# Performance work log

Measured on AMD Instinct MI355X. Metric: run time of the kernel, lower is better.

The kernel has to match this reference:

```python
import jax, jax.numpy as jnp
import numpy as np

EPSILON = 0.1       # temperature
ITERATIONS = 10     # Sinkhorn iterations


def setup_inputs() -> dict:
    key = jax.random.key(0)
    z = jax.random.normal(key, (8192, 128), dtype=jnp.float32)  # [2N, D]
    return {"z": z}


def reference(z):
    # L2-normalize rows; cosine similarity of normalized rows is a plain matmul
    z = z / jnp.linalg.norm(z, axis=1, keepdims=True)
    cos_sim = z @ z.T                      # [S, S]
    Cost = 1.0 - cos_sim
    S = Cost.shape[0]
    C = Cost.max()
    eye = jnp.eye(S, dtype=Cost.dtype)
    Cost = C * eye + (1.0 - eye) * Cost    # put max cost on the diagonal
    Probs = jnp.exp(-Cost / EPSILON)
    for _ in range(ITERATIONS):
        Probs = Probs / Probs.sum(axis=1, keepdims=True)   # row normalize
        Probs = (Probs / Probs.sum(axis=0, keepdims=True)).T  # col normalize + transpose (as in source)
    N = S // 2
    Probi = jnp.diagonal(Probs, offset=N)   # positives view1->view2
    Probj = jnp.diagonal(Probs, offset=-N)  # positives view2->view1
    L = -(jnp.log(Probi).sum() + jnp.log(Probj).sum()) / (2 * N)
    return L
```

## Files before the change

kernel.cpp:

```cpp
#include <hip/hip_runtime.h>

#define S_DIM 8192
#define NTRI 2080
#define NWORK 544

typedef __attribute__((ext_vector_type(8))) short short8v;
typedef __attribute__((ext_vector_type(16))) float f32x16;
typedef __attribute__((ext_vector_type(2))) float f32x2;

__device__ inline unsigned short f32_to_bf16(float f) {
    unsigned int b = __builtin_bit_cast(unsigned int, f);
    unsigned int lsb = (b >> 16) & 1u;
    b += 0x7fffu + lsb;
    return (unsigned short)(b >> 16);
}
__device__ inline unsigned int fkey(float f) {
    unsigned int b = __builtin_bit_cast(unsigned int, f);
    return (b & 0x80000000u) ? ~b : (b | 0x80000000u);
}
__device__ inline float fkey_inv(unsigned int k) {
    unsigned int b = (k & 0x80000000u) ? (k & 0x7FFFFFFFu) : ~k;
    return __builtin_bit_cast(float, b);
}

__device__ inline unsigned int f32_to_fp8_scalar(float f) {
#if __has_builtin(__builtin_amdgcn_cvt_pk_fp8_f32)
    return (unsigned int)__builtin_amdgcn_cvt_pk_fp8_f32(f, f, 0, false) & 0xFFu;
#else
    if (f < 0.015625f) return (unsigned int)__float2int_rn(f * 512.0f);
    unsigned int b = __builtin_bit_cast(unsigned int, f);
    unsigned int r = b + 0x7FFFFu + ((b >> 20) & 1u);
    return (r >> 20) - 960u;
#endif
}
__device__ inline unsigned int pack_fp8x4(float a, float b, float c, float d) {
#if __has_builtin(__builtin_amdgcn_cvt_pk_fp8_f32)
    int w = __builtin_amdgcn_cvt_pk_fp8_f32(a, b, 0, false);
    w = __builtin_amdgcn_cvt_pk_fp8_f32(c, d, w, true);
    return (unsigned int)w;
#else
    return f32_to_fp8_scalar(a) | (f32_to_fp8_scalar(b) << 8) |
           (f32_to_fp8_scalar(c) << 16) | (f32_to_fp8_scalar(d) << 24);
#endif
}
#if !__has_builtin(__builtin_amdgcn_cvt_pk_f32_fp8)
__device__ inline float fp8_byte_to_f32(unsigned int u) {
    unsigned int e = (u >> 3) & 15u, m = u & 7u;
    if (e == 0) return (float)m * 0x1p-9f;
    return __builtin_bit_cast(float, ((e + 120u) << 23) | (m << 20));
}
#endif
__device__ inline void fp8x4_to_f32(unsigned int d, float* o) {
#if __has_builtin(__builtin_amdgcn_cvt_pk_f32_fp8)
    f32x2 lo = __builtin_amdgcn_cvt_pk_f32_fp8((int)d, false);
    f32x2 hi = __builtin_amdgcn_cvt_pk_f32_fp8((int)d, true);
    o[0] = lo[0]; o[1] = lo[1]; o[2] = hi[0]; o[3] = hi[1];
#else
    o[0] = fp8_byte_to_f32(d & 0xFFu);
    o[1] = fp8_byte_to_f32((d >> 8) & 0xFFu);
    o[2] = fp8_byte_to_f32((d >> 16) & 0xFFu);
    o[3] = fp8_byte_to_f32((d >> 24) & 0xFFu);
#endif
}

__device__ inline void tri_map(int id, int& bi, int& bj) {
    int j = (int)((sqrtf(8.0f * (float)id + 1.0f) - 1.0f) * 0.5f);
    while ((j + 1) * (j + 2) / 2 <= id) ++j;
    while (j * (j + 1) / 2 > id) --j;
    bj = j;
    bi = id - j * (j + 1) / 2;
}
__device__ inline void work_map(int id, int& R, int& s) {
    int g = (int)((sqrtf(1.0f + 2.0f * (float)id) - 1.0f) * 0.5f);
    while (2 * (g + 1) * (g + 2) <= id) ++g;
    while (2 * g * (g + 1) > id) --g;
    int rem = id - 2 * g * (g + 1);
    int r = rem / (g + 1);
    s = rem - r * (g + 1);
    R = 4 * g + r;
}

__global__ __launch_bounds__(64) void normalize_kernel(const float* __restrict__ z,
                                                       unsigned int* __restrict__ znb,
                                                       float* __restrict__ y0,
                                                       float* __restrict__ y1,
                                                       unsigned int* __restrict__ minslot,
                                                       float* __restrict__ lossacc,
                                                       unsigned int* __restrict__ cnt) {
    int row = blockIdx.x;
    int t = threadIdx.x;
    float2 val = ((const float2*)(z + (size_t)row * 128))[t];
    float ss = val.x * val.x + val.y * val.y;
    #pragma unroll
    for (int off = 32; off; off >>= 1) ss += __shfl_xor(ss, off);
    float inv = 1.0f / sqrtf(ss);
    float2 o; o.x = val.x * inv; o.y = val.y * inv;
    unsigned int pk = (unsigned int)f32_to_bf16(o.x) | ((unsigned int)f32_to_bf16(o.y) << 16);
    znb[((row >> 5) * 512 + (t >> 2) * 32 + (row & 31)) * 4 + (t & 3)] = pk;
    if (t == 0) {
        y0[row] = 1.0f;
        y1[row] = 0.0f;
        if (row == 0) { *minslot = 0xFFFFFFFFu; *lossacc = 0.0f; *cnt = 0u; }
    }
}

__global__ __launch_bounds__(512, 4) void gemm_exp_mfma(const short* __restrict__ znb,
                                                        unsigned char* __restrict__ K8,
                                                        unsigned int* __restrict__ minslot,
                                                        float* __restrict__ lossacc) {
    __shared__ unsigned int Tl[128 * 32];
    __shared__ float wmins[8];
    int bi, bj;
    tri_map(blockIdx.x, bi, bj);
    const bool pairblk = (bj - bi == 32);
    const bool diagblk = (bi == bj);
    const int t = threadIdx.x;
    const int lane = t & 63, w = t >> 6;
    const int tr = w >> 1, tc = w & 1;
    const int cl = lane & 31, hi = lane >> 5;
    const int rowA = bi * 128 + tr * 32;
    const short8v* Z = (const short8v*)znb;

    f32x16 acc[2];
    #pragma unroll
    for (int tj = 0; tj < 2; ++tj)
        #pragma unroll
        for (int e = 0; e < 16; ++e) acc[tj][e] = 0.0f;

    #pragma unroll
    for (int step = 0; step < 8; ++step) {
        const int chunk = step * 2 + hi;
        short8v af = Z[(rowA >> 5) * 512 + chunk * 32 + cl];
        short8v bf[2];
        #pragma unroll
        for (int tj = 0; tj < 2; ++tj) {
            int rB = bj * 128 + tc * 64 + tj * 32;
            bf[tj] = Z[(rB >> 5) * 512 + chunk * 32 + cl];
        }
        #pragma unroll
        for (int tj = 0; tj < 2; ++tj)
            acc[tj] = __builtin_amdgcn_mfma_f32_32x32x16_bf16(af, bf[tj], acc[tj], 0, 0, 0);
    }

    float mn = 3.0e38f;
    float pl = 0.0f;
    #pragma unroll
    for (int tj = 0; tj < 2; ++tj) {
        int colL = tc * 64 + tj * 32 + cl;
        int colG = bj * 128 + colL;
        int gswz = ((colL & 15) << 1) | ((colL >> 3) & 1);
        #pragma unroll
        for (int g = 0; g < 4; ++g) {
            int rowG = rowA + 8 * g + 4 * hi;
            float ev[4];
            #pragma unroll
            for (int kk = 0; kk < 4; ++kk) {
                float c = acc[tj][g * 4 + kk];
                mn = fminf(mn, c);
                if (pairblk && (colG - rowG - kk) == 4096) pl += 20.0f * (c - 1.0f);
                ev[kk] = __expf(10.0f * fminf(c, 0.6f));
            }
            if (diagblk) {
                #pragma unroll
                for (int kk = 0; kk < 4; ++kk)
                    if (rowG + kk == colG) ev[kk] = 0.0f;
            }
            unsigned int wv = pack_fp8x4(ev[0], ev[1], ev[2], ev[3]);
            int r4b = tr * 8 + 2 * g + hi;
            Tl[colL * 32 + (r4b ^ gswz)] = wv;
        }
    }
    #pragma unroll
    for (int off = 32; off; off >>= 1) mn = fminf(mn, __shfl_xor(mn, off));
    if (lane == 0) wmins[w] = mn;
    if (pairblk) {
        #pragma unroll
        for (int off = 32; off; off >>= 1) pl += __shfl_xor(pl, off);
        if (lane == 0) atomicAdd(lossacc, pl);
    }
    __syncthreads();
    if (t == 0) {
        float bmin = wmins[0];
        #pragma unroll
        for (int k = 1; k < 8; ++k) bmin = fminf(bmin, wmins[k]);
        atomicMin(minslot, fkey(bmin));
    }

    const size_t gbase = (size_t)(bj * 128) * S_DIM + (size_t)bi * 128;
    #pragma unroll
    for (int it = 0; it < 2; ++it) {
        int c = it * 64 + (t >> 3);
        int dq = (t & 7) * 4;
        int g2 = ((c & 15) << 1) | ((c >> 3) & 1);
        uint4 wv;
        wv.x = Tl[c * 32 + ((dq + 0) ^ g2)];
        wv.y = Tl[c * 32 + ((dq + 1) ^ g2)];
        wv.z = Tl[c * 32 + ((dq + 2) ^ g2)];
        wv.w = Tl[c * 32 + ((dq + 3) ^ g2)];
        *(uint4*)(K8 + gbase + (size_t)c * S_DIM + dq * 4) = wv;
    }
}

__global__ __launch_bounds__(256, 3) void sink_pass_kernel(const unsigned char* __restrict__ K8,
                                                           const float* __restrict__ yprev,
                                                           float* __restrict__ ycur,
                                                           float* __restrict__ ynext,
                                                           const unsigned int* __restrict__ minslot) {
    __shared__ float xsc[512];
    __shared__ float xsr[128];
    __shared__ float rdp[128 * 33];
    __shared__ float csum[4 * 512];
    const int t = threadIdx.x;
    const int id = blockIdx.x;
    if (id < 32) ynext[id * 256 + t] = 0.0f;

    int R, s;
    work_map(id, R, s);
    const int q0 = s * 4;
    if (t < 128) xsr[t] = 1.0f / yprev[R * 128 + t];
    xsc[t]       = 1.0f / yprev[q0 * 128 + t];
    xsc[t + 256] = 1.0f / yprev[q0 * 128 + 256 + t];

    const int w = t >> 6, lane = t & 63, half = lane >> 5, d = lane & 31;
    const int C = q0 + (d >> 3);
    const bool tvalid = (C <= R);
    const bool cvalid = (C < R);

    uint4 kreg[16];
    const unsigned char* base = K8 + (size_t)(R * 128) * S_DIM + q0 * 128 + d * 16
                                   + (size_t)((w << 5) + half) * S_DIM;
    if (tvalid) {
        #pragma unroll
        for (int i2 = 0; i2 < 16; ++i2)
            kreg[i2] = *(const uint4*)(base + (size_t)(i2 << 1) * S_DIM);
    } else {
        #pragma unroll
        for (int i2 = 0; i2 < 16; ++i2) kreg[i2] = (uint4){0u, 0u, 0u, 0u};
    }
    __syncthreads();

    float xr[16];
    #pragma unroll
    for (int u = 0; u < 4; ++u)
        *(float4*)&xr[u * 4] = *(const float4*)&xsc[d * 16 + u * 4];
    float ca[16];
    #pragma unroll
    for (int e = 0; e < 16; ++e) ca[e] = 0.0f;

    #pragma unroll
    for (int i2 = 0; i2 < 16; ++i2) {
        int row = (w << 5) + (i2 << 1) + half;
        float f[16];
        fp8x4_to_f32(kreg[i2].x, f + 0);  fp8x4_to_f32(kreg[i2].y, f + 4);
        fp8x4_to_f32(kreg[i2].z, f + 8);  fp8x4_to_f32(kreg[i2].w, f + 12);
        float rd = 0.0f;
        #pragma unroll
        for (int e = 0; e < 16; ++e) rd += f[e] * xr[e];
        if (cvalid) {
            float xv = xsr[row];
            #pragma unroll
            for (int e = 0; e < 16; ++e) ca[e] += f[e] * xv;
        }
        rdp[row * 33 + d] = rd;
    }
    #pragma unroll
    for (int e = 0; e < 16; ++e) ca[e] += __shfl_xor(ca[e], 32);
    if (half == 0) {
        #pragma unroll
        for (int u = 0; u < 4; ++u) {
            float4 v; v.x = ca[u*4]; v.y = ca[u*4+1]; v.z = ca[u*4+2]; v.w = ca[u*4+3];
            *(float4*)&csum[w * 512 + d * 16 + u * 4] = v;
        }
    }
    __syncthreads();
    if (t < 128) {
        float sum = 0.0f;
        #pragma unroll
        for (int k = 0; k < 32; ++k) sum += rdp[t * 33 + k];
        if (s == (R >> 2))
            sum += __expf(10.0f * fkey_inv(*minslot)) * xsr[t];
        atomicAdd(&ycur[R * 128 + t], sum);
    }
    #pragma unroll
    for (int u = 0; u < 2; ++u) {
        int cc = t + u * 256;
        int Cc = q0 + (cc >> 7);
        if (Cc < R)
            atomicAdd(&ycur[q0 * 128 + cc],
                      csum[cc] + csum[512 + cc] + csum[1024 + cc] + csum[1536 + cc]);
    }
}

__global__ __launch_bounds__(256) void loss_kernel(const float* __restrict__ y11,
                                                   const float* __restrict__ y10,
                                                   float* __restrict__ lossacc,
                                                   unsigned int* __restrict__ cnt,
                                                   float* __restrict__ out) {
    __shared__ float wpart[4];
    const int t = threadIdx.x;
    int i = blockIdx.x * 256 + t;
    float val = 10.0f - __logf(y11[i]) - __logf(y10[i]);
    #pragma unroll
    for (int off = 32; off; off >>= 1) val += __shfl_xor(val, off);
    if ((t & 63) == 0) wpart[t >> 6] = val;
    __syncthreads();
    if (t == 0) {
        atomicAdd(lossacc, wpart[0] + wpart[1] + wpart[2] + wpart[3]);
        __threadfence();
        unsigned int done = atomicAdd(cnt, 1u);
        if (done == gridDim.x - 1) {
            __threadfence();
            out[0] = -(*(volatile float*)lossacc) / (float)S_DIM;
        }
    }
}

extern "C" void kernel_launch(void* const* d_in, const int* in_sizes, int n_in,
                              void* d_out, int out_size, void* d_ws, size_t ws_size,
                              hipStream_t stream) {
    const float* z = (const float*)d_in[0];
    float* out = (float*)d_out;
    char* ws = (char*)d_ws;

    unsigned int* znb  = (unsigned int*)ws;
    float* y0          = (float*)(ws + (2 << 20));
    float* y1          = (float*)(ws + (2 << 20) + 65536);
    float* y2          = (float*)(ws + (2 << 20) + 131072);
    unsigned int* mins = (unsigned int*)(ws + (2 << 20) + 196608);
    float* lossacc     = (float*)(ws + (2 << 20) + 196608 + 64);
    unsigned int* cnt  = (unsigned int*)(ws + (2 << 20) + 196608 + 128);
    unsigned char* K8  = (unsigned char*)(ws + (8 << 20));

    float* ybuf[3] = {y0, y1, y2};

    normalize_kernel<<<S_DIM, 64, 0, stream>>>(z, znb, y0, y1, mins, lossacc, cnt);
    gemm_exp_mfma<<<NTRI, 512, 0, stream>>>((const short*)znb, K8, mins, lossacc);

    for (int p = 1; p <= 11; ++p)
        sink_pass_kernel<<<NWORK, 256, 0, stream>>>(K8, ybuf[(p - 1) % 3], ybuf[p % 3],
                                                    ybuf[(p + 1) % 3], mins);

    loss_kernel<<<S_DIM / 256, 256, 0, stream>>>(y2, y1, lossacc, cnt, out);
}
```

Baseline: 148.0 us.

## Fuse first Sinkhorn pass row/col sums into GEMM-exp epilogue

The GEMM-exp kernel now computes the first pass's row and column sums of the fp8 kernel tile directly from shared memory and atomically accumulates them into y1. The diagonal term is added via an offset in the next pass. This removes one of the eleven sink_pass launches, along with its full read of the 64MB fp8 matrix. In exchange it adds epilogue work and atomics to the GEMM kernel, and the per-lane loops over LDS may bank-conflict.

```diff
diff --git a/kernel.cpp b/kernel.cpp
--- a/kernel.cpp
+++ b/kernel.cpp
@@ -43,13 +43,11 @@
            (f32_to_fp8_scalar(c) << 16) | (f32_to_fp8_scalar(d) << 24);
 #endif
 }
-#if !__has_builtin(__builtin_amdgcn_cvt_pk_f32_fp8)
 __device__ inline float fp8_byte_to_f32(unsigned int u) {
     unsigned int e = (u >> 3) & 15u, m = u & 7u;
     if (e == 0) return (float)m * 0x1p-9f;
     return __builtin_bit_cast(float, ((e + 120u) << 23) | (m << 20));
 }
-#endif
 __device__ inline void fp8x4_to_f32(unsigned int d, float* o) {
 #if __has_builtin(__builtin_amdgcn_cvt_pk_f32_fp8)
     f32x2 lo = __builtin_amdgcn_cvt_pk_f32_fp8((int)d, false);
@@ -82,8 +80,8 @@
 
 __global__ __launch_bounds__(64) void normalize_kernel(const float* __restrict__ z,
                                                        unsigned int* __restrict__ znb,
-                                                       float* __restrict__ y0,
                                                        float* __restrict__ y1,
+                                                       float* __restrict__ y2,
                                                        unsigned int* __restrict__ minslot,
                                                        float* __restrict__ lossacc,
                                                        unsigned int* __restrict__ cnt) {
@@ -98,8 +96,8 @@
     unsigned int pk = (unsigned int)f32_to_bf16(o.x) | ((unsigned int)f32_to_bf16(o.y) << 16);
     znb[((row >> 5) * 512 + (t >> 2) * 32 + (row & 31)) * 4 + (t & 3)] = pk;
     if (t == 0) {
-        y0[row] = 1.0f;
         y1[row] = 0.0f;
+        y2[row] = 0.0f;
         if (row == 0) { *minslot = 0xFFFFFFFFu; *lossacc = 0.0f; *cnt = 0u; }
     }
 }
@@ -107,7 +105,8 @@
 __global__ __launch_bounds__(512, 4) void gemm_exp_mfma(const short* __restrict__ znb,
                                                         unsigned char* __restrict__ K8,
                                                         unsigned int* __restrict__ minslot,
-                                                        float* __restrict__ lossacc) {
+                                                        float* __restrict__ lossacc,
+                                                        float* __restrict__ y1) {
     __shared__ unsigned int Tl[128 * 32];
     __shared__ float wmins[8];
     int bi, bj;
@@ -199,13 +198,40 @@
         wv.w = Tl[c * 32 + ((dq + 3) ^ g2)];
         *(uint4*)(K8 + gbase + (size_t)c * S_DIM + dq * 4) = wv;
     }
+
+    if (t < 128) {
+        if (!diagblk) {
+            int c = t;
+            float sum = 0.0f;
+            #pragma unroll
+            for (int j = 0; j < 32; ++j) {
+                unsigned int dw = Tl[c * 32 + ((j + c) & 31)];
+                float f[4];
+                fp8x4_to_f32(dw, f);
+                sum += (f[0] + f[1]) + (f[2] + f[3]);
+            }
+            atomicAdd(&y1[bj * 128 + c], sum);
+        }
+    } else if (t < 256) {
+        int r = t - 128;
+        int r4 = r >> 2, k8 = (r & 3) * 8;
+        float sum = 0.0f;
+        #pragma unroll 8
+        for (int c = 0; c < 128; ++c) {
+            int g2 = ((c & 15) << 1) | ((c >> 3) & 1);
+            unsigned int dw = Tl[c * 32 + (r4 ^ g2)];
+            sum += fp8_byte_to_f32((dw >> k8) & 0xFFu);
+        }
+        atomicAdd(&y1[bi * 128 + r], sum);
+    }
 }
 
 __global__ __launch_bounds__(256, 3) void sink_pass_kernel(const unsigned char* __restrict__ K8,
                                                            const float* __restrict__ yprev,
                                                            float* __restrict__ ycur,
                                                            float* __restrict__ ynext,
-                                                           const unsigned int* __restrict__ minslot) {
+                                                           const unsigned int* __restrict__ minslot,
+                                                           int addkd) {
     __shared__ float xsc[512];
     __shared__ float xsr[128];
     __shared__ float rdp[128 * 33];
@@ -217,9 +243,11 @@
     int R, s;
     work_map(id, R, s);
     const int q0 = s * 4;
-    if (t < 128) xsr[t] = 1.0f / yprev[R * 128 + t];
-    xsc[t]       = 1.0f / yprev[q0 * 128 + t];
-    xsc[t + 256] = 1.0f / yprev[q0 * 128 + 256 + t];
+    const float kd = __expf(10.0f * fkey_inv(*minslot));
+    const float ofs = addkd ? kd : 0.0f;
+    if (t < 128) xsr[t] = 1.0f / (yprev[R * 128 + t] + ofs);
+    xsc[t]       = 1.0f / (yprev[q0 * 128 + t] + ofs);
+    xsc[t + 256] = 1.0f / (yprev[q0 * 128 + 256 + t] + ofs);
 
     const int w = t >> 6, lane = t & 63, half = lane >> 5, d = lane & 31;
     const int C = q0 + (d >> 3);
@@ -278,7 +306,7 @@
         #pragma unroll
         for (int k = 0; k < 32; ++k) sum += rdp[t * 33 + k];
         if (s == (R >> 2))
-            sum += __expf(10.0f * fkey_inv(*minslot)) * xsr[t];
+            sum += kd * xsr[t];
         atomicAdd(&ycur[R * 128 + t], sum);
     }
     #pragma unroll
@@ -333,12 +361,12 @@
 
     float* ybuf[3] = {y0, y1, y2};
 
-    normalize_kernel<<<S_DIM, 64, 0, stream>>>(z, znb, y0, y1, mins, lossacc, cnt);
-    gemm_exp_mfma<<<NTRI, 512, 0, stream>>>((const short*)znb, K8, mins, lossacc);
-
-    for (int p = 1; p <= 11; ++p)
+    normalize_kernel<<<S_DIM, 64, 0, stream>>>(z, znb, y1, y2, mins, lossacc, cnt);
+    gemm_exp_mfma<<<NTRI, 512, 0, stream>>>((const short*)znb, K8, mins, lossacc, y1);
+
+    for (int p = 2; p <= 11; ++p)
         sink_pass_kernel<<<NWORK, 256, 0, stream>>>(K8, ybuf[(p - 1) % 3], ybuf[p % 3],
-                                                    ybuf[(p + 1) % 3], mins);
+                                                    ybuf[(p + 1) % 3], mins, (p == 2) ? 1 : 0);
 
     loss_kernel<<<S_DIM / 256, 256, 0, stream>>>(y2, y1, lossacc, cnt, out);
 }
```

New measurement: 153.7 us. 3.9% more time.
